# Kernel tuning notes

Hardware: AMD Instinct MI355X
Metric: run time of the kernel (lower is better)

The kernel has to match this reference:

```python
import jax, jax.numpy as jnp
import numpy as np

N = 100000      # nodes
E = 3200000     # edges
F_IN = 512
HID = 16
C = 10


def setup_inputs() -> dict:
    key = jax.random.key(0)
    k1, k2, k3, k4 = jax.random.split(key, 4)
    x = jax.random.normal(k1, (N, F_IN), dtype=jnp.float32)
    edge_index = jax.random.randint(k2, (2, E), 0, N, dtype=jnp.int64)
    W1 = jax.random.normal(k3, (F_IN, HID), dtype=jnp.float32) * 0.05
    b1 = jnp.zeros((HID,), dtype=jnp.float32)
    W2 = jax.random.normal(k4, (HID, C), dtype=jnp.float32) * 0.05
    b2 = jnp.zeros((C,), dtype=jnp.float32)
    return {"x": x, "edge_index": edge_index, "W1": W1, "b1": b1, "W2": W2, "b2": b2}


def _gcn_norm(edge_index, n):
    # add self-loops, compute symmetric normalization deg^-1/2 * deg^-1/2
    loops = jnp.arange(n, dtype=edge_index.dtype)
    src = jnp.concatenate([edge_index[0], loops])
    dst = jnp.concatenate([edge_index[1], loops])
    deg = jax.ops.segment_sum(jnp.ones_like(dst, dtype=jnp.float32), dst, num_segments=n)
    dinv = jnp.where(deg > 0, jax.lax.rsqrt(deg), 0.0)
    norm = dinv[src] * dinv[dst]  # [E+N]
    return src, dst, norm


def _gcn_layer(h, W, b, src, dst, norm, n):
    h = h @ W                                   # project first (PyG GCNConv)
    msg = h[src] * norm[:, None]                # gather + edge scaling
    agg = jax.ops.segment_sum(msg, dst, num_segments=n)  # scatter-add
    return agg + b


def reference(x, edge_index, W1, b1, W2, b2):
    n = x.shape[0]
    src, dst, norm = _gcn_norm(edge_index, n)
    h = jax.nn.relu(_gcn_layer(x, W1, b1, src, dst, norm, n))
    # F.dropout with training=False is identity (eval mode)
    out = _gcn_layer(h, W2, b2, src, dst, norm, n)
    return jax.nn.log_softmax(out, axis=1)
```

## Files before the change

kernel.cpp:

```cpp
#include <hip/hip_runtime.h>
#include <hip/hip_fp16.h>

#define N_NODES 100000
#define N_EDGES 3200000
#define F_IN    512
#define HID     16
#define NCLS    10
#define NB      196
#define EPB     4096
#define TK      32

union H2F { __half2 h; float f; };
__device__ __forceinline__ float h2f_pack(float a, float b) {
    H2F u; u.h = __floats2half2_rn(a, b); return u.f;
}
__device__ __forceinline__ void h2f_add(float raw, float& a, float& b) {
    H2F u; u.f = raw; float2 v = __half22float2(u.h); a += v.x; b += v.y;
}
__device__ __forceinline__ void acc4(float2 raw, float& a, float& b, float& c, float& d) {
    h2f_add(raw.x, a, b); h2f_add(raw.y, c, d);
}

__global__ __launch_bounds__(256) void k_binit(int* __restrict__ bcntp) {
    int i = blockIdx.x * 256 + threadIdx.x;
    if (i < NB * 16) bcntp[i] = 0;
}

__global__ __launch_bounds__(256) void k_bhist(const int* __restrict__ dst,
                                               int* __restrict__ bcntp) {
    __shared__ int h[256];
    int t = threadIdx.x;
    h[t] = 0;
    __syncthreads();
    int hi = min(N_EDGES, (int)(blockIdx.x + 1) * 8192);
    for (int e = blockIdx.x * 8192 + t; e < hi; e += 256)
        atomicAdd(&h[dst[e] >> 9], 1);
    __syncthreads();
    if (t < NB) {
        int v = h[t];
        if (v) atomicAdd(&bcntp[t * 16], v);
    }
}

__global__ __launch_bounds__(256) void k_bscan(const int* __restrict__ bcntp,
                                               int* __restrict__ boff,
                                               int* __restrict__ bcurp,
                                               int* __restrict__ row) {
    __shared__ int sh[256];
    int t = threadIdx.x;
    int v = (t < NB) ? bcntp[t * 16] : 0;
    sh[t] = v;
    __syncthreads();
    for (int off = 1; off < 256; off <<= 1) {
        int add = (t >= off) ? sh[t - off] : 0;
        __syncthreads();
        sh[t] += add;
        __syncthreads();
    }
    int excl = sh[t] - v;
    if (t < NB) { boff[t] = excl; bcurp[t * 16] = excl; }
    if (t == 0) { boff[NB] = N_EDGES; row[N_NODES] = N_EDGES; }
}

__global__ __launch_bounds__(256) void k_bpart(const int* __restrict__ ei,
                                               int* __restrict__ bcurp,
                                               int* __restrict__ part) {
    __shared__ int cnt_sh[256], base_sh[256];
    int t = threadIdx.x;
    cnt_sh[t] = 0;
    __syncthreads();
    int base = blockIdx.x * EPB;
    int pk[16], bk[16], rk[16];
#pragma unroll
    for (int j = 0; j < 16; ++j) {
        int e = base + j * 256 + t;
        if (e < N_EDGES) {
            int s = ei[e], d = ei[N_EDGES + e];
            bk[j] = d >> 9;
            pk[j] = ((d & 511) << 17) | s;
            rk[j] = atomicAdd(&cnt_sh[bk[j]], 1);
        } else bk[j] = -1;
    }
    __syncthreads();
    if (t < NB && cnt_sh[t] > 0)
        base_sh[t] = atomicAdd(&bcurp[t * 16], cnt_sh[t]);
    __syncthreads();
#pragma unroll
    for (int j = 0; j < 16; ++j)
        if (bk[j] >= 0) part[base_sh[bk[j]] + rk[j]] = pk[j];
}

__global__ __launch_bounds__(256) void k_bucket(const int* __restrict__ boff,
                                                const int* __restrict__ part,
                                                int* __restrict__ row,
                                                float* __restrict__ dinv,
                                                int* __restrict__ srcs) {
    __shared__ int cnt[512], ofs[512], sc[256];
    int t = threadIdx.x;
    int b = blockIdx.x;
    int e0 = boff[b], e1 = boff[b + 1];
    int nbase = b << 9;
    cnt[t] = 0; cnt[t + 256] = 0;
    __syncthreads();
    for (int e = e0 + t; e < e1; e += 1024) {
        int p0 = part[e];
        int p1 = (e + 256 < e1) ? part[e + 256] : -1;
        int p2 = (e + 512 < e1) ? part[e + 512] : -1;
        int p3 = (e + 768 < e1) ? part[e + 768] : -1;
        atomicAdd(&cnt[p0 >> 17], 1);
        if (p1 >= 0) atomicAdd(&cnt[p1 >> 17], 1);
        if (p2 >= 0) atomicAdd(&cnt[p2 >> 17], 1);
        if (p3 >= 0) atomicAdd(&cnt[p3 >> 17], 1);
    }
    __syncthreads();
    int a0 = cnt[2 * t], a1 = cnt[2 * t + 1];
    sc[t] = a0 + a1;
    __syncthreads();
    for (int off = 1; off < 256; off <<= 1) {
        int add = (t >= off) ? sc[t - off] : 0;
        __syncthreads();
        sc[t] += add;
        __syncthreads();
    }
    int excl = sc[t] - (a0 + a1);
    ofs[2 * t] = excl;
    ofs[2 * t + 1] = excl + a0;
    __syncthreads();
#pragma unroll
    for (int r = 0; r < 2; ++r) {
        int ln = t + r * 256;
        int n = nbase + ln;
        if (n < N_NODES) {
            row[n] = e0 + ofs[ln];
            dinv[n] = rsqrtf((float)(cnt[ln] + 1));
        }
    }
    __syncthreads();
    for (int e = e0 + t; e < e1; e += 1024) {
        int p0 = part[e];
        int p1 = (e + 256 < e1) ? part[e + 256] : -1;
        int p2 = (e + 512 < e1) ? part[e + 512] : -1;
        int p3 = (e + 768 < e1) ? part[e + 768] : -1;
        int o0 = atomicAdd(&ofs[p0 >> 17], 1);
        srcs[e0 + o0] = p0 & 0x1FFFF;
        if (p1 >= 0) { int o = atomicAdd(&ofs[p1 >> 17], 1); srcs[e0 + o] = p1 & 0x1FFFF; }
        if (p2 >= 0) { int o = atomicAdd(&ofs[p2 >> 17], 1); srcs[e0 + o] = p2 & 0x1FFFF; }
        if (p3 >= 0) { int o = atomicAdd(&ofs[p3 >> 17], 1); srcs[e0 + o] = p3 & 0x1FFFF; }
    }
}

__global__ __launch_bounds__(128) void k_gemm1(const float* __restrict__ x,
                                               const float* __restrict__ W1,
                                               const float* __restrict__ dinv,
                                               __half* __restrict__ h1h) {
    __shared__ float xs[128][TK + 1];
    __shared__ float wchunk[TK * 16];
    const int t = threadIdx.x;
    const int nbase = blockIdx.x * 128;
    const int f4 = t & 7;
    const int r0 = t >> 3;

    float4 pre[8];
#pragma unroll
    for (int p = 0; p < 8; ++p) {
        int n = nbase + r0 + p * 16;
        pre[p] = (n < N_NODES) ? ((const float4*)(x + (size_t)n * F_IN))[f4]
                               : make_float4(0.f, 0.f, 0.f, 0.f);
    }
    float4 wpre = ((const float4*)W1)[t];

    float acc[16];
#pragma unroll
    for (int j = 0; j < 16; ++j) acc[j] = 0.f;

    for (int c = 0; c < F_IN; c += TK) {
#pragma unroll
        for (int p = 0; p < 8; ++p) {
            int r = r0 + p * 16;
            xs[r][f4 * 4 + 0] = pre[p].x;
            xs[r][f4 * 4 + 1] = pre[p].y;
            xs[r][f4 * 4 + 2] = pre[p].z;
            xs[r][f4 * 4 + 3] = pre[p].w;
        }
        ((float4*)wchunk)[t] = wpre;
        __syncthreads();
        if (c + TK < F_IN) {
#pragma unroll
            for (int p = 0; p < 8; ++p) {
                int n = nbase + r0 + p * 16;
                pre[p] = (n < N_NODES)
                           ? ((const float4*)(x + (size_t)n * F_IN + c + TK))[f4]
                           : make_float4(0.f, 0.f, 0.f, 0.f);
            }
            wpre = ((const float4*)(W1 + (c + TK) * 16))[t];
        }
#pragma unroll
        for (int k = 0; k < TK; ++k) {
            float xv = xs[t][k];
            const float4* wk = (const float4*)&wchunk[k * 16];
            float4 wa = wk[0], wb = wk[1], wc = wk[2], wd = wk[3];
            acc[0]  = fmaf(xv, wa.x, acc[0]);
            acc[1]  = fmaf(xv, wa.y, acc[1]);
            acc[2]  = fmaf(xv, wa.z, acc[2]);
            acc[3]  = fmaf(xv, wa.w, acc[3]);
            acc[4]  = fmaf(xv, wb.x, acc[4]);
            acc[5]  = fmaf(xv, wb.y, acc[5]);
            acc[6]  = fmaf(xv, wb.z, acc[6]);
            acc[7]  = fmaf(xv, wb.w, acc[7]);
            acc[8]  = fmaf(xv, wc.x, acc[8]);
            acc[9]  = fmaf(xv, wc.y, acc[9]);
            acc[10] = fmaf(xv, wc.z, acc[10]);
            acc[11] = fmaf(xv, wc.w, acc[11]);
            acc[12] = fmaf(xv, wd.x, acc[12]);
            acc[13] = fmaf(xv, wd.y, acc[13]);
            acc[14] = fmaf(xv, wd.z, acc[14]);
            acc[15] = fmaf(xv, wd.w, acc[15]);
        }
        __syncthreads();
    }

    int n = nbase + t;
    if (n < N_NODES) {
        float dn = dinv[n];
        float4 o0 = make_float4(h2f_pack(acc[0]  * dn, acc[1]  * dn),
                                h2f_pack(acc[2]  * dn, acc[3]  * dn),
                                h2f_pack(acc[4]  * dn, acc[5]  * dn),
                                h2f_pack(acc[6]  * dn, acc[7]  * dn));
        float4 o1 = make_float4(h2f_pack(acc[8]  * dn, acc[9]  * dn),
                                h2f_pack(acc[10] * dn, acc[11] * dn),
                                h2f_pack(acc[12] * dn, acc[13] * dn),
                                h2f_pack(acc[14] * dn, acc[15] * dn));
        float4* o = (float4*)(h1h + (size_t)n * 16);
        o[0] = o0; o[1] = o1;
    }
}

__global__ __launch_bounds__(256) void k_edge1f(const int* __restrict__ row,
                                                const int* __restrict__ srcs,
                                                const float* __restrict__ dinv,
                                                const __half* __restrict__ h1h,
                                                const float* __restrict__ b1,
                                                const float* __restrict__ W2,
                                                __half* __restrict__ ps) {
    __shared__ float w2s[HID * NCLS];
    if (threadIdx.x < HID * NCLS) w2s[threadIdx.x] = W2[threadIdx.x];
    __syncthreads();
    int t = blockIdx.x * 256 + threadIdx.x;
    if (t >= N_NODES * 4) return;
    int n = t >> 2, q = t & 3;
    const float2* h2 = (const float2*)h1h;
    float s0 = 0.f, s1 = 0.f, s2 = 0.f, s3 = 0.f;
    acc4(h2[n * 4 + q], s0, s1, s2, s3);
    int k = row[n], k1 = row[n + 1];
    for (; k + 8 <= k1; k += 8) {
        int a0 = srcs[k],     a1 = srcs[k + 1], a2 = srcs[k + 2], a3 = srcs[k + 3];
        int a4 = srcs[k + 4], a5 = srcs[k + 5], a6 = srcs[k + 6], a7 = srcs[k + 7];
        float2 v0 = h2[a0 * 4 + q], v1 = h2[a1 * 4 + q];
        float2 v2 = h2[a2 * 4 + q], v3 = h2[a3 * 4 + q];
        float2 v4 = h2[a4 * 4 + q], v5 = h2[a5 * 4 + q];
        float2 v6 = h2[a6 * 4 + q], v7 = h2[a7 * 4 + q];
        acc4(v0, s0, s1, s2, s3); acc4(v1, s0, s1, s2, s3);
        acc4(v2, s0, s1, s2, s3); acc4(v3, s0, s1, s2, s3);
        acc4(v4, s0, s1, s2, s3); acc4(v5, s0, s1, s2, s3);
        acc4(v6, s0, s1, s2, s3); acc4(v7, s0, s1, s2, s3);
    }
    if (k < k1) {
        int sb = srcs[k];
        int idx[8]; float2 vv[8];
#pragma unroll
        for (int j = 0; j < 8; ++j) idx[j] = (k + j < k1) ? srcs[k + j] : sb;
#pragma unroll
        for (int j = 0; j < 8; ++j) vv[j] = h2[idx[j] * 4 + q];
#pragma unroll
        for (int j = 0; j < 8; ++j)
            if (k + j < k1) acc4(vv[j], s0, s1, s2, s3);
    }
    float dn = dinv[n];
    int c0 = q * 4;
    float r0 = fmaxf(fmaf(dn, s0, b1[c0 + 0]), 0.f);
    float r1 = fmaxf(fmaf(dn, s1, b1[c0 + 1]), 0.f);
    float r2 = fmaxf(fmaf(dn, s2, b1[c0 + 2]), 0.f);
    float r3 = fmaxf(fmaf(dn, s3, b1[c0 + 3]), 0.f);
    float p[NCLS];
#pragma unroll
    for (int c = 0; c < NCLS; ++c)
        p[c] = r0 * w2s[(c0 + 0) * NCLS + c] + r1 * w2s[(c0 + 1) * NCLS + c]
             + r2 * w2s[(c0 + 2) * NCLS + c] + r3 * w2s[(c0 + 3) * NCLS + c];
#pragma unroll
    for (int c = 0; c < NCLS; ++c) {
        p[c] += __shfl_xor(p[c], 1);
        p[c] += __shfl_xor(p[c], 2);
    }
    float o0, o1, o2, o3;
    if (q == 0)      { o0 = p[0]; o1 = p[1]; o2 = p[2]; o3 = p[3]; }
    else if (q == 1) { o0 = p[4]; o1 = p[5]; o2 = p[6]; o3 = p[7]; }
    else if (q == 2) { o0 = p[8]; o1 = p[9]; o2 = 0.f;  o3 = 0.f;  }
    else             { o0 = 0.f;  o1 = 0.f;  o2 = 0.f;  o3 = 0.f;  }
    float2 st = make_float2(h2f_pack(o0 * dn, o1 * dn), h2f_pack(o2 * dn, o3 * dn));
    ((float2*)ps)[n * 4 + q] = st;
}

__global__ __launch_bounds__(256) void k_edge2f(const int* __restrict__ row,
                                                const int* __restrict__ srcs,
                                                const float* __restrict__ dinv,
                                                const __half* __restrict__ ps,
                                                const float* __restrict__ b2,
                                                float* __restrict__ out) {
    int t = blockIdx.x * 256 + threadIdx.x;
    if (t >= N_NODES * 4) return;
    int n = t >> 2, q = t & 3;
    const float2* p2 = (const float2*)ps;
    float s0 = 0.f, s1 = 0.f, s2 = 0.f, s3 = 0.f;
    acc4(p2[n * 4 + q], s0, s1, s2, s3);
    int k = row[n], k1 = row[n + 1];
    for (; k + 8 <= k1; k += 8) {
        int a0 = srcs[k],     a1 = srcs[k + 1], a2 = srcs[k + 2], a3 = srcs[k + 3];
        int a4 = srcs[k + 4], a5 = srcs[k + 5], a6 = srcs[k + 6], a7 = srcs[k + 7];
        float2 v0 = p2[a0 * 4 + q], v1 = p2[a1 * 4 + q];
        float2 v2 = p2[a2 * 4 + q], v3 = p2[a3 * 4 + q];
        float2 v4 = p2[a4 * 4 + q], v5 = p2[a5 * 4 + q];
        float2 v6 = p2[a6 * 4 + q], v7 = p2[a7 * 4 + q];
        acc4(v0, s0, s1, s2, s3); acc4(v1, s0, s1, s2, s3);
        acc4(v2, s0, s1, s2, s3); acc4(v3, s0, s1, s2, s3);
        acc4(v4, s0, s1, s2, s3); acc4(v5, s0, s1, s2, s3);
        acc4(v6, s0, s1, s2, s3); acc4(v7, s0, s1, s2, s3);
    }
    if (k < k1) {
        int sb = srcs[k];
        int idx[8]; float2 vv[8];
#pragma unroll
        for (int j = 0; j < 8; ++j) idx[j] = (k + j < k1) ? srcs[k + j] : sb;
#pragma unroll
        for (int j = 0; j < 8; ++j) vv[j] = p2[idx[j] * 4 + q];
#pragma unroll
        for (int j = 0; j < 8; ++j)
            if (k + j < k1) acc4(vv[j], s0, s1, s2, s3);
    }
    float dn = dinv[n];
    int c0 = q * 4;
    float v0 = (c0 + 0 < NCLS) ? fmaf(dn, s0, b2[c0 + 0]) : -1e30f;
    float v1 = (c0 + 1 < NCLS) ? fmaf(dn, s1, b2[c0 + 1]) : -1e30f;
    float v2 = (c0 + 2 < NCLS) ? fmaf(dn, s2, b2[c0 + 2]) : -1e30f;
    float v3 = (c0 + 3 < NCLS) ? fmaf(dn, s3, b2[c0 + 3]) : -1e30f;
    float m = fmaxf(fmaxf(v0, v1), fmaxf(v2, v3));
    m = fmaxf(m, __shfl_xor(m, 1));
    m = fmaxf(m, __shfl_xor(m, 2));
    float se = __expf(v0 - m) + __expf(v1 - m) + __expf(v2 - m) + __expf(v3 - m);
    se += __shfl_xor(se, 1);
    se += __shfl_xor(se, 2);
    float l = m + __logf(se);
    if (q < 2) {
        float* o = out + n * NCLS + c0;
        o[0] = v0 - l; o[1] = v1 - l; o[2] = v2 - l; o[3] = v3 - l;
    } else if (q == 2) {
        float* o = out + n * NCLS + 8;
        o[0] = v0 - l; o[1] = v1 - l;
    }
}

extern "C" void kernel_launch(void* const* d_in, const int* in_sizes, int n_in,
                              void* d_out, int out_size, void* d_ws, size_t ws_size,
                              hipStream_t stream) {
    const float* x  = (const float*)d_in[0];
    const int*   ei = (const int*)d_in[1];
    const float* W1 = (const float*)d_in[2];
    const float* b1 = (const float*)d_in[3];
    const float* W2 = (const float*)d_in[4];
    const float* b2 = (const float*)d_in[5];
    float* out = (float*)d_out;

    int* w = (int*)d_ws;
    float*  dinv  = (float*)w;
    int*    row   = w + 102400;
    int*    bcntp = w + 204816;
    int*    bcurp = w + 207952;
    int*    boff  = w + 211088;
    int*    part  = w + 211344;
    int*    srcs  = w + 3411344;
    __half* h1h   = (__half*)(w + 6611344);
    __half* ps    = (__half*)(w + 9888144);

    k_binit<<<(NB * 16 + 255) / 256, 256, 0, stream>>>(bcntp);
    k_bhist<<<(N_EDGES + 8191) / 8192, 256, 0, stream>>>(ei + N_EDGES, bcntp);
    k_bscan<<<1, 256, 0, stream>>>(bcntp, boff, bcurp, row);
    k_bpart<<<(N_EDGES + EPB - 1) / EPB, 256, 0, stream>>>(ei, bcurp, part);
    k_bucket<<<NB, 256, 0, stream>>>(boff, part, row, dinv, srcs);

    k_gemm1 <<<(N_NODES + 127) / 128, 128, 0, stream>>>(x, W1, dinv, h1h);
    k_edge1f<<<(N_NODES * 4 + 255) / 256, 256, 0, stream>>>(row, srcs, dinv, h1h, b1, W2, ps);
    k_edge2f<<<(N_NODES * 4 + 255) / 256, 256, 0, stream>>>(row, srcs, dinv, ps, b2, out);
}
```

Before: 454.4 us.

## Vectorize edge loads, widen bucket blocks, deepen gather unroll, memset init

Edge index loads in the histogram and partition kernels now use int4 vector loads. The per-bucket CSR builder runs with 1024 threads and does a single 512-wide scan instead of a paired 256-wide one. Both aggregation kernels gather 16 neighbours per iteration instead of 8 to raise memory-level parallelism, at the cost of more registers and a longer masked tail. The zero-init kernel is replaced with hipMemsetAsync.

New measurement: 436.0 us (median of 2 runs). -4.0%, faster.

```diff
diff --git a/kernel.cpp b/kernel.cpp
--- a/kernel.cpp
+++ b/kernel.cpp
@@ -21,20 +21,21 @@
     h2f_add(raw.x, a, b); h2f_add(raw.y, c, d);
 }
 
-__global__ __launch_bounds__(256) void k_binit(int* __restrict__ bcntp) {
-    int i = blockIdx.x * 256 + threadIdx.x;
-    if (i < NB * 16) bcntp[i] = 0;
-}
-
-__global__ __launch_bounds__(256) void k_bhist(const int* __restrict__ dst,
+__global__ __launch_bounds__(256) void k_bhist(const int4* __restrict__ dst4,
                                                int* __restrict__ bcntp) {
     __shared__ int h[256];
     int t = threadIdx.x;
     h[t] = 0;
     __syncthreads();
-    int hi = min(N_EDGES, (int)(blockIdx.x + 1) * 8192);
-    for (int e = blockIdx.x * 8192 + t; e < hi; e += 256)
-        atomicAdd(&h[dst[e] >> 9], 1);
+    int base4 = blockIdx.x * 2048;
+    int hi4 = min(N_EDGES / 4, base4 + 2048);
+    for (int e4 = base4 + t; e4 < hi4; e4 += 256) {
+        int4 d = dst4[e4];
+        atomicAdd(&h[d.x >> 9], 1);
+        atomicAdd(&h[d.y >> 9], 1);
+        atomicAdd(&h[d.z >> 9], 1);
+        atomicAdd(&h[d.w >> 9], 1);
+    }
     __syncthreads();
     if (t < NB) {
         int v = h[t];
@@ -69,17 +70,27 @@
     int t = threadIdx.x;
     cnt_sh[t] = 0;
     __syncthreads();
-    int base = blockIdx.x * EPB;
+    const int4* s4 = (const int4*)ei;
+    const int4* d4 = (const int4*)(ei + N_EDGES);
+    int base4 = blockIdx.x * 1024;
     int pk[16], bk[16], rk[16];
 #pragma unroll
-    for (int j = 0; j < 16; ++j) {
-        int e = base + j * 256 + t;
-        if (e < N_EDGES) {
-            int s = ei[e], d = ei[N_EDGES + e];
-            bk[j] = d >> 9;
-            pk[j] = ((d & 511) << 17) | s;
-            rk[j] = atomicAdd(&cnt_sh[bk[j]], 1);
-        } else bk[j] = -1;
+    for (int j = 0; j < 4; ++j) {
+        int e4 = base4 + j * 256 + t;
+        if (e4 < N_EDGES / 4) {
+            int4 s = s4[e4], d = d4[e4];
+            bk[4 * j + 0] = d.x >> 9; pk[4 * j + 0] = ((d.x & 511) << 17) | s.x;
+            bk[4 * j + 1] = d.y >> 9; pk[4 * j + 1] = ((d.y & 511) << 17) | s.y;
+            bk[4 * j + 2] = d.z >> 9; pk[4 * j + 2] = ((d.z & 511) << 17) | s.z;
+            bk[4 * j + 3] = d.w >> 9; pk[4 * j + 3] = ((d.w & 511) << 17) | s.w;
+            rk[4 * j + 0] = atomicAdd(&cnt_sh[bk[4 * j + 0]], 1);
+            rk[4 * j + 1] = atomicAdd(&cnt_sh[bk[4 * j + 1]], 1);
+            rk[4 * j + 2] = atomicAdd(&cnt_sh[bk[4 * j + 2]], 1);
+            rk[4 * j + 3] = atomicAdd(&cnt_sh[bk[4 * j + 3]], 1);
+        } else {
+            bk[4 * j + 0] = -1; bk[4 * j + 1] = -1;
+            bk[4 * j + 2] = -1; bk[4 * j + 3] = -1;
+        }
     }
     __syncthreads();
     if (t < NB && cnt_sh[t] > 0)
@@ -90,57 +101,54 @@
         if (bk[j] >= 0) part[base_sh[bk[j]] + rk[j]] = pk[j];
 }
 
-__global__ __launch_bounds__(256) void k_bucket(const int* __restrict__ boff,
-                                                const int* __restrict__ part,
-                                                int* __restrict__ row,
-                                                float* __restrict__ dinv,
-                                                int* __restrict__ srcs) {
-    __shared__ int cnt[512], ofs[512], sc[256];
+__global__ __launch_bounds__(1024) void k_bucket(const int* __restrict__ boff,
+                                                 const int* __restrict__ part,
+                                                 int* __restrict__ row,
+                                                 float* __restrict__ dinv,
+                                                 int* __restrict__ srcs) {
+    __shared__ int cnt[512], ofs[512];
     int t = threadIdx.x;
     int b = blockIdx.x;
     int e0 = boff[b], e1 = boff[b + 1];
     int nbase = b << 9;
-    cnt[t] = 0; cnt[t + 256] = 0;
-    __syncthreads();
-    for (int e = e0 + t; e < e1; e += 1024) {
+    if (t < 512) cnt[t] = 0;
+    __syncthreads();
+    for (int e = e0 + t; e < e1; e += 4096) {
         int p0 = part[e];
-        int p1 = (e + 256 < e1) ? part[e + 256] : -1;
-        int p2 = (e + 512 < e1) ? part[e + 512] : -1;
-        int p3 = (e + 768 < e1) ? part[e + 768] : -1;
+        int p1 = (e + 1024 < e1) ? part[e + 1024] : -1;
+        int p2 = (e + 2048 < e1) ? part[e + 2048] : -1;
+        int p3 = (e + 3072 < e1) ? part[e + 3072] : -1;
         atomicAdd(&cnt[p0 >> 17], 1);
         if (p1 >= 0) atomicAdd(&cnt[p1 >> 17], 1);
         if (p2 >= 0) atomicAdd(&cnt[p2 >> 17], 1);
         if (p3 >= 0) atomicAdd(&cnt[p3 >> 17], 1);
     }
     __syncthreads();
-    int a0 = cnt[2 * t], a1 = cnt[2 * t + 1];
-    sc[t] = a0 + a1;
-    __syncthreads();
-    for (int off = 1; off < 256; off <<= 1) {
-        int add = (t >= off) ? sc[t - off] : 0;
-        __syncthreads();
-        sc[t] += add;
-        __syncthreads();
-    }
-    int excl = sc[t] - (a0 + a1);
-    ofs[2 * t] = excl;
-    ofs[2 * t + 1] = excl + a0;
-    __syncthreads();
-#pragma unroll
-    for (int r = 0; r < 2; ++r) {
-        int ln = t + r * 256;
-        int n = nbase + ln;
+    int v = (t < 512) ? cnt[t] : 0;
+    if (t < 512) ofs[t] = v;
+    __syncthreads();
+    for (int off = 1; off < 512; off <<= 1) {
+        int add = (t >= off && t < 512) ? ofs[t - off] : 0;
+        __syncthreads();
+        if (t < 512) ofs[t] += add;
+        __syncthreads();
+    }
+    int excl = (t < 512) ? (ofs[t] - v) : 0;
+    __syncthreads();
+    if (t < 512) {
+        ofs[t] = excl;
+        int n = nbase + t;
         if (n < N_NODES) {
-            row[n] = e0 + ofs[ln];
-            dinv[n] = rsqrtf((float)(cnt[ln] + 1));
-        }
-    }
-    __syncthreads();
-    for (int e = e0 + t; e < e1; e += 1024) {
+            row[n] = e0 + excl;
+            dinv[n] = rsqrtf((float)(v + 1));
+        }
+    }
+    __syncthreads();
+    for (int e = e0 + t; e < e1; e += 4096) {
         int p0 = part[e];
-        int p1 = (e + 256 < e1) ? part[e + 256] : -1;
-        int p2 = (e + 512 < e1) ? part[e + 512] : -1;
-        int p3 = (e + 768 < e1) ? part[e + 768] : -1;
+        int p1 = (e + 1024 < e1) ? part[e + 1024] : -1;
+        int p2 = (e + 2048 < e1) ? part[e + 2048] : -1;
+        int p3 = (e + 3072 < e1) ? part[e + 3072] : -1;
         int o0 = atomicAdd(&ofs[p0 >> 17], 1);
         srcs[e0 + o0] = p0 & 0x1FFFF;
         if (p1 >= 0) { int o = atomicAdd(&ofs[p1 >> 17], 1); srcs[e0 + o] = p1 & 0x1FFFF; }
@@ -252,28 +260,27 @@
     float s0 = 0.f, s1 = 0.f, s2 = 0.f, s3 = 0.f;
     acc4(h2[n * 4 + q], s0, s1, s2, s3);
     int k = row[n], k1 = row[n + 1];
-    for (; k + 8 <= k1; k += 8) {
-        int a0 = srcs[k],     a1 = srcs[k + 1], a2 = srcs[k + 2], a3 = srcs[k + 3];
-        int a4 = srcs[k + 4], a5 = srcs[k + 5], a6 = srcs[k + 6], a7 = srcs[k + 7];
-        float2 v0 = h2[a0 * 4 + q], v1 = h2[a1 * 4 + q];
-        float2 v2 = h2[a2 * 4 + q], v3 = h2[a3 * 4 + q];
-        float2 v4 = h2[a4 * 4 + q], v5 = h2[a5 * 4 + q];
-        float2 v6 = h2[a6 * 4 + q], v7 = h2[a7 * 4 + q];
-        acc4(v0, s0, s1, s2, s3); acc4(v1, s0, s1, s2, s3);
-        acc4(v2, s0, s1, s2, s3); acc4(v3, s0, s1, s2, s3);
-        acc4(v4, s0, s1, s2, s3); acc4(v5, s0, s1, s2, s3);
-        acc4(v6, s0, s1, s2, s3); acc4(v7, s0, s1, s2, s3);
+    for (; k + 16 <= k1; k += 16) {
+        int a[16];
+#pragma unroll
+        for (int j = 0; j < 16; ++j) a[j] = srcs[k + j];
+        float2 v[16];
+#pragma unroll
+        for (int j = 0; j < 16; ++j) v[j] = h2[a[j] * 4 + q];
+#pragma unroll
+        for (int j = 0; j < 16; ++j) acc4(v[j], s0, s1, s2, s3);
     }
     if (k < k1) {
         int sb = srcs[k];
-        int idx[8]; float2 vv[8];
-#pragma unroll
-        for (int j = 0; j < 8; ++j) idx[j] = (k + j < k1) ? srcs[k + j] : sb;
-#pragma unroll
-        for (int j = 0; j < 8; ++j) vv[j] = h2[idx[j] * 4 + q];
-#pragma unroll
-        for (int j = 0; j < 8; ++j)
-            if (k + j < k1) acc4(vv[j], s0, s1, s2, s3);
+        int a[16];
+#pragma unroll
+        for (int j = 0; j < 16; ++j) a[j] = (k + j < k1) ? srcs[k + j] : sb;
+        float2 v[16];
+#pragma unroll
+        for (int j = 0; j < 16; ++j) v[j] = h2[a[j] * 4 + q];
+#pragma unroll
+        for (int j = 0; j < 16; ++j)
+            if (k + j < k1) acc4(v[j], s0, s1, s2, s3);
     }
     float dn = dinv[n];
     int c0 = q * 4;
@@ -313,28 +320,27 @@
     float s0 = 0.f, s1 = 0.f, s2 = 0.f, s3 = 0.f;
     acc4(p2[n * 4 + q], s0, s1, s2, s3);
     int k = row[n], k1 = row[n + 1];
-    for (; k + 8 <= k1; k += 8) {
-        int a0 = srcs[k],     a1 = srcs[k + 1], a2 = srcs[k + 2], a3 = srcs[k + 3];
-        int a4 = srcs[k + 4], a5 = srcs[k + 5], a6 = srcs[k + 6], a7 = srcs[k + 7];
-        float2 v0 = p2[a0 * 4 + q], v1 = p2[a1 * 4 + q];
-        float2 v2 = p2[a2 * 4 + q], v3 = p2[a3 * 4 + q];
-        float2 v4 = p2[a4 * 4 + q], v5 = p2[a5 * 4 + q];
-        float2 v6 = p2[a6 * 4 + q], v7 = p2[a7 * 4 + q];
-        acc4(v0, s0, s1, s2, s3); acc4(v1, s0, s1, s2, s3);
-        acc4(v2, s0, s1, s2, s3); acc4(v3, s0, s1, s2, s3);
-        acc4(v4, s0, s1, s2, s3); acc4(v5, s0, s1, s2, s3);
-        acc4(v6, s0, s1, s2, s3); acc4(v7, s0, s1, s2, s3);
+    for (; k + 16 <= k1; k += 16) {
+        int a[16];
+#pragma unroll
+        for (int j = 0; j < 16; ++j) a[j] = srcs[k + j];
+        float2 v[16];
+#pragma unroll
+        for (int j = 0; j < 16; ++j) v[j] = p2[a[j] * 4 + q];
+#pragma unroll
+        for (int j = 0; j < 16; ++j) acc4(v[j], s0, s1, s2, s3);
     }
     if (k < k1) {
         int sb = srcs[k];
-        int idx[8]; float2 vv[8];
-#pragma unroll
-        for (int j = 0; j < 8; ++j) idx[j] = (k + j < k1) ? srcs[k + j] : sb;
-#pragma unroll
-        for (int j = 0; j < 8; ++j) vv[j] = p2[idx[j] * 4 + q];
-#pragma unroll
-        for (int j = 0; j < 8; ++j)
-            if (k + j < k1) acc4(vv[j], s0, s1, s2, s3);
+        int a[16];
+#pragma unroll
+        for (int j = 0; j < 16; ++j) a[j] = (k + j < k1) ? srcs[k + j] : sb;
+        float2 v[16];
+#pragma unroll
+        for (int j = 0; j < 16; ++j) v[j] = p2[a[j] * 4 + q];
+#pragma unroll
+        for (int j = 0; j < 16; ++j)
+            if (k + j < k1) acc4(v[j], s0, s1, s2, s3);
     }
     float dn = dinv[n];
     int c0 = q * 4;
@@ -380,11 +386,11 @@
     __half* h1h   = (__half*)(w + 6611344);
     __half* ps    = (__half*)(w + 9888144);
 
-    k_binit<<<(NB * 16 + 255) / 256, 256, 0, stream>>>(bcntp);
-    k_bhist<<<(N_EDGES + 8191) / 8192, 256, 0, stream>>>(ei + N_EDGES, bcntp);
+    hipMemsetAsync(bcntp, 0, NB * 16 * sizeof(int), stream);
+    k_bhist<<<(N_EDGES + 8191) / 8192, 256, 0, stream>>>((const int4*)(ei + N_EDGES), bcntp);
     k_bscan<<<1, 256, 0, stream>>>(bcntp, boff, bcurp, row);
     k_bpart<<<(N_EDGES + EPB - 1) / EPB, 256, 0, stream>>>(ei, bcurp, part);
-    k_bucket<<<NB, 256, 0, stream>>>(boff, part, row, dinv, srcs);
+    k_bucket<<<NB, 1024, 0, stream>>>(boff, part, row, dinv, srcs);
 
     k_gemm1 <<<(N_NODES + 127) / 128, 128, 0, stream>>>(x, W1, dinv, h1h);
     k_edge1f<<<(N_NODES * 4 + 255) / 256, 256, 0, stream>>>(row, srcs, dinv, h1h, b1, W2, ps);
```
